# Performance work log

Hardware: AMD Instinct MI355X
Metric: run time of the kernel (lower is better)

Reference implementation:

```python
import jax, jax.numpy as jnp
import numpy as np

B, T, C, H = 2, 2048, 1024, 16
D = C // H  # head_dim = 64

def setup_inputs() -> dict:
    key = jax.random.key(0)
    k0, k1, k2, k3, k4 = jax.random.split(key, 5)
    s = 1.0 / np.sqrt(C)
    return {
        "x": jax.random.normal(k0, (B, T, C), dtype=jnp.float32),
        "w_qkv": jax.random.uniform(k1, (C, 3 * C), jnp.float32, -s, s),
        "b_qkv": jax.random.uniform(k2, (3 * C,), jnp.float32, -s, s),
        "w_proj": jax.random.uniform(k3, (C, C), jnp.float32, -s, s),
        "b_proj": jax.random.uniform(k4, (C,), jnp.float32, -s, s),
    }

def reference(x, w_qkv, b_qkv, w_proj, b_proj):
    Bx, Tx, Cx = x.shape
    qkv = x @ w_qkv + b_qkv                      # [B,T,3C]
    q, k, v = jnp.split(qkv, 3, axis=-1)
    # [B,T,C] -> [B,H,T,D]
    def heads(t):
        return t.reshape(Bx, Tx, H, D).transpose(0, 2, 1, 3)
    q, k, v = heads(q), heads(k), heads(v)
    att = jnp.einsum('bhqd,bhkd->bhqk', q, k) / np.sqrt(D).astype(np.float32)
    causal = jnp.tril(jnp.ones((Tx, Tx), dtype=bool))
    att = jnp.where(causal, att, -jnp.inf)
    att = jax.nn.softmax(att, axis=-1)
    y = jnp.einsum('bhqk,bhkd->bhqd', att, v)    # [B,H,T,D]
    y = y.transpose(0, 2, 1, 3).reshape(Bx, Tx, Cx)
    return y @ w_proj + b_proj
```

## Files before the change

kernel.cpp:

```cpp
#include <hip/hip_runtime.h>

typedef short bf16x8 __attribute__((ext_vector_type(8)));
typedef float f32x4 __attribute__((ext_vector_type(4)));
typedef unsigned short u16;
typedef unsigned short u16x8 __attribute__((ext_vector_type(8)));
typedef unsigned short u16x4 __attribute__((ext_vector_type(4), may_alias));

__device__ __forceinline__ u16 f2bf(float f) {
    union { float f; unsigned u; } v; v.f = f;
    unsigned r = v.u + 0x7fffu + ((v.u >> 16) & 1u);
    return (u16)(r >> 16);
}
__device__ __forceinline__ u16 f2bf_rhu(float f) {
    union { float f; unsigned u; } v; v.f = f;
    return (u16)((v.u + 0x8000u) >> 16);
}

__device__ __forceinline__ void gld_lds16(const void* g, void* l) {
    __builtin_amdgcn_global_load_lds(
        (const __attribute__((address_space(1))) void*)g,
        (__attribute__((address_space(3))) void*)l, 16, 0, 0);
}

__global__ __launch_bounds__(256) void x_to_bf16(const float* __restrict__ in,
                                                 u16* __restrict__ out) {
    const int i = blockIdx.x * 256 + threadIdx.x;
    float4 a = ((const float4*)in)[i * 2];
    float4 b = ((const float4*)in)[i * 2 + 1];
    u16x8 h;
    h[0] = f2bf(a.x); h[1] = f2bf(a.y); h[2] = f2bf(a.z); h[3] = f2bf(a.w);
    h[4] = f2bf(b.x); h[5] = f2bf(b.y); h[6] = f2bf(b.z); h[7] = f2bf(b.w);
    *(u16x8*)(out + (size_t)i * 8) = h;
}

__global__ __launch_bounds__(256) void transpose_w(const float* __restrict__ in,
                                                   u16* __restrict__ out,
                                                   int K, int N) {
    __shared__ float tile[32][33];
    const int n0 = blockIdx.x * 32, k0 = blockIdx.y * 32;
    const int tx = threadIdx.x, ty = threadIdx.y;
#pragma unroll
    for (int i = 0; i < 32; i += 8)
        tile[ty + i][tx] = in[(size_t)(k0 + ty + i) * N + n0 + tx];
    __syncthreads();
#pragma unroll
    for (int i = 0; i < 32; i += 8)
        out[(size_t)(n0 + ty + i) * K + k0 + tx] = f2bf(tile[tx][ty + i]);
}

#define QSCALE 0.180336880f

template <int OUTMODE, int BN>
__global__ __launch_bounds__(256) void gemm_m97(
    const u16* __restrict__ A, const u16* __restrict__ Bt,
    const float* __restrict__ bias, float* __restrict__ Cf,
    u16* __restrict__ Qo, u16* __restrict__ Ko, u16* __restrict__ Vt,
    int M, int N, int K) {
    constexpr int NF = BN / 32;
    __shared__ __align__(16) u16 lA[128 * 64];
    __shared__ __align__(16) u16 lB[BN * 64];

    const int tid = threadIdx.x;
    const int lane = tid & 63, wid = tid >> 6;
    const int wr = wid >> 1, wc = wid & 1;
    const int fr = lane & 15, fq = lane >> 4;
    const int m0 = blockIdx.y * 128, n0 = blockIdx.x * BN;

    const int gsrc = (lane & 7) ^ (lane >> 3);
    const u16* gA0 = A + (size_t)(m0 + (tid >> 3)) * K + gsrc * 8;
    const u16* gB0 = Bt + (size_t)(n0 + (tid >> 3)) * K + gsrc * 8;
    u16* lAw = lA + wid * 512;
    u16* lBw = lB + wid * 512;

    const int r7 = fr & 7;
    const int gk[2] = { ((0 + fq) ^ r7) * 8, ((4 + fq) ^ r7) * 8 };

    f32x4 acc[4][NF];
#pragma unroll
    for (int m = 0; m < 4; m++)
#pragma unroll
        for (int n = 0; n < NF; n++)
#pragma unroll
            for (int r = 0; r < 4; r++) acc[m][n][r] = 0.f;

    for (int k0 = 0; k0 < K; k0 += 64) {
        __syncthreads();
#pragma unroll
        for (int c = 0; c < 4; c++)
            gld_lds16(gA0 + (size_t)(c * 32) * K + k0, lAw + c * 2048);
#pragma unroll
        for (int c = 0; c < BN / 32; c++)
            gld_lds16(gB0 + (size_t)(c * 32) * K + k0, lBw + c * 2048);
        __syncthreads();

#pragma unroll
        for (int kf = 0; kf < 2; kf++) {
            bf16x8 a[4], b[NF];
#pragma unroll
            for (int m = 0; m < 4; m++)
                a[m] = *(const bf16x8*)&lA[(wr * 64 + m * 16 + fr) * 64 + gk[kf]];
#pragma unroll
            for (int n = 0; n < NF; n++)
                b[n] = *(const bf16x8*)&lB[(wc * (BN / 2) + n * 16 + fr) * 64 + gk[kf]];
#pragma unroll
            for (int m = 0; m < 4; m++)
#pragma unroll
                for (int n = 0; n < NF; n++)
                    acc[m][n] = __builtin_amdgcn_mfma_f32_16x16x32_bf16(a[m], b[n], acc[m][n], 0, 0, 0);
        }
    }

#pragma unroll
    for (int m = 0; m < 4; m++) {
#pragma unroll
        for (int n = 0; n < NF; n++) {
            const int row0 = m0 + wr * 64 + m * 16 + fq * 4;
            const int col = n0 + wc * (BN / 2) + n * 16 + fr;
            float v4[4];
#pragma unroll
            for (int r = 0; r < 4; r++) v4[r] = acc[m][n][r] + bias[col];
            if (OUTMODE == 0) {
                const int bb = row0 >> 11, t0 = row0 & 2047;
                const int sec = col >> 10, cc = col & 1023;
                const int h = cc >> 6, d = cc & 63;
                if (sec == 0) {
#pragma unroll
                    for (int r = 0; r < 4; r++)
                        Qo[(((size_t)(bb * 16 + h) * 2048 + t0 + r) << 6) + d] = f2bf(v4[r] * QSCALE);
                } else if (sec == 1) {
#pragma unroll
                    for (int r = 0; r < 4; r++)
                        Ko[(((size_t)(bb * 16 + h) * 2048 + t0 + r) << 6) + d] = f2bf(v4[r]);
                } else {
                    ushort4 p;
                    p.x = f2bf(v4[0]); p.y = f2bf(v4[1]); p.z = f2bf(v4[2]); p.w = f2bf(v4[3]);
                    *(ushort4*)&Vt[(((size_t)(bb * 16 + h) * 64 + d) << 11) + t0] = p;
                }
            } else {
#pragma unroll
                for (int r = 0; r < 4; r++)
                    Cf[(size_t)(row0 + r) * N + col] = v4[r];
            }
        }
    }
}

__global__ __launch_bounds__(256) void attn_kernel(const u16* __restrict__ Q,
                                                   const u16* __restrict__ Kg,
                                                   const u16* __restrict__ Vt,
                                                   u16* __restrict__ O) {
    __shared__ __align__(16) u16 lK[2][64 * 64];
    __shared__ __align__(16) u16 lV[2][64 * 64];
    __shared__ __align__(16) u16 lP[4][16 * 64];

    const int tid = threadIdx.x;
    const int lane = tid & 63, wid = tid >> 6;
    const int fr = lane & 15, fq = lane >> 4;
    const int bh = blockIdx.x & 31;
    const int qi = 31 - (blockIdx.x >> 5);
    const int qb0 = qi * 64;
    const size_t base = (size_t)bh * (2048 * 64);
    const u16* Qp = Q + base;
    const u16* Kp = Kg + base;
    const u16* Vp = Vt + base;

    const int q0 = qb0 + wid * 16;
    bf16x8 qa[2];
#pragma unroll
    for (int kf = 0; kf < 2; kf++)
        qa[kf] = *(const bf16x8*)&Qp[(size_t)(q0 + fr) * 64 + kf * 32 + fq * 8];
    asm volatile("s_waitcnt vmcnt(0)" ::: "memory");

    bf16x8 vones;
#pragma unroll
    for (int j = 0; j < 8; j++) vones[j] = (short)0x3F80;

    f32x4 o[4], lsum;
#pragma unroll
    for (int r = 0; r < 4; r++) {
        lsum[r] = 0.f;
#pragma unroll
        for (int n = 0; n < 4; n++) o[n][r] = 0.f;
    }

    const int srow0 = wid * 8 + (lane >> 3);
    const int gsrc = (lane & 7) ^ (lane >> 3);
    const u16* kSrc0 = Kp + (size_t)srow0 * 64 + gsrc * 8;
    const u16* vSrc0 = Vp + ((size_t)srow0 << 11) + gsrc * 8;

    const int r7 = fr & 7;
    const int gk0 = ((0 + fq) ^ r7) * 8;
    const int gk1 = ((4 + fq) ^ r7) * 8;

    const int pw_base = fr * 64 + (fq & 1) * 4;
    const int pw_gx = (fq >> 1);

    const int nt = qi + 1;

#define STAGE(buf, kt0_)                                                        \
    do {                                                                        \
        const int _kt0 = (kt0_);                                                \
        u16* _lkw = &lK[buf][wid * 512];                                        \
        u16* _lvw = &lV[buf][wid * 512];                                        \
        gld_lds16(kSrc0 + (size_t)_kt0 * 64, _lkw);                             \
        gld_lds16(kSrc0 + (size_t)(_kt0 + 32) * 64, _lkw + 2048);               \
        gld_lds16(vSrc0 + _kt0, _lvw);                                          \
        gld_lds16(vSrc0 + ((size_t)32 << 11) + _kt0, _lvw + 2048);              \
    } while (0)

    STAGE(0, 0);

    for (int kt = 0; kt < nt; kt++) {
        const int cur = kt & 1;
        if (kt + 1 < nt) {
            STAGE(cur ^ 1, (kt + 1) << 6);
            asm volatile("s_waitcnt vmcnt(4)" ::: "memory");
        } else {
            asm volatile("s_waitcnt vmcnt(0)" ::: "memory");
        }
        __builtin_amdgcn_s_barrier();

        const int kt0 = kt << 6;
        const u16* lKc = lK[cur];
        const u16* lVc = lV[cur];

        f32x4 s[4];
#pragma unroll
        for (int n = 0; n < 4; n++)
#pragma unroll
            for (int r = 0; r < 4; r++) s[n][r] = 0.f;
        __builtin_amdgcn_s_setprio(1);
#pragma unroll
        for (int n = 0; n < 4; n++) {
            bf16x8 kb0 = *(const bf16x8*)&lKc[(n * 16 + fr) * 64 + gk0];
            bf16x8 kb1 = *(const bf16x8*)&lKc[(n * 16 + fr) * 64 + gk1];
            s[n] = __builtin_amdgcn_mfma_f32_16x16x32_bf16(kb0, qa[0], s[n], 0, 0, 0);
            s[n] = __builtin_amdgcn_mfma_f32_16x16x32_bf16(kb1, qa[1], s[n], 0, 0, 0);
        }
        __builtin_amdgcn_s_setprio(0);

        if (kt == nt - 1) {
            const int qg = q0 + fr;
#pragma unroll
            for (int n = 0; n < 4; n++) {
                const int kg0 = kt0 + n * 16 + fq * 4;
#pragma unroll
                for (int r = 0; r < 4; r++)
                    if (kg0 + r > qg) s[n][r] = -200.f;
            }
        }

#pragma unroll
        for (int n = 0; n < 4; n++) {
            u16x4 w;
            w[0] = f2bf_rhu(__builtin_amdgcn_exp2f(s[n][0]));
            w[1] = f2bf_rhu(__builtin_amdgcn_exp2f(s[n][1]));
            w[2] = f2bf_rhu(__builtin_amdgcn_exp2f(s[n][2]));
            w[3] = f2bf_rhu(__builtin_amdgcn_exp2f(s[n][3]));
            const int g = ((2 * n + pw_gx) ^ r7) * 8;
            *(u16x4*)&lP[wid][pw_base + g] = w;
        }
        asm volatile("" ::: "memory");

        __builtin_amdgcn_s_setprio(1);
#pragma unroll
        for (int kf = 0; kf < 2; kf++) {
            const int gv = (kf == 0) ? gk0 : gk1;
            bf16x8 pb = *(const bf16x8*)&lP[wid][fr * 64 + gv];
            lsum = __builtin_amdgcn_mfma_f32_16x16x32_bf16(vones, pb, lsum, 0, 0, 0);
#pragma unroll
            for (int n = 0; n < 4; n++) {
                bf16x8 va = *(const bf16x8*)&lVc[(n * 16 + fr) * 64 + gv];
                o[n] = __builtin_amdgcn_mfma_f32_16x16x32_bf16(va, pb, o[n], 0, 0, 0);
            }
        }
        __builtin_amdgcn_s_setprio(0);

        __builtin_amdgcn_s_barrier();
    }
#undef STAGE

    const int bb = bh >> 4, hh = bh & 15;
    const float inv = 1.f / lsum[0];
    u16* orow = O + ((size_t)(bb * 2048 + q0 + fr)) * 1024 + hh * 64 + fq * 4;
#pragma unroll
    for (int n = 0; n < 4; n++) {
        ushort4 h;
        h.x = f2bf(o[n][0] * inv);
        h.y = f2bf(o[n][1] * inv);
        h.z = f2bf(o[n][2] * inv);
        h.w = f2bf(o[n][3] * inv);
        *(ushort4*)&orow[n * 16] = h;
    }
}

extern "C" void kernel_launch(void* const* d_in, const int* in_sizes, int n_in,
                              void* d_out, int out_size, void* d_ws, size_t ws_size,
                              hipStream_t stream) {
    const float* x      = (const float*)d_in[0];
    const float* w_qkv  = (const float*)d_in[1];
    const float* b_qkv  = (const float*)d_in[2];
    const float* w_proj = (const float*)d_in[3];
    const float* b_proj = (const float*)d_in[4];
    float* out = (float*)d_out;

    u16* ws = (u16*)d_ws;
    u16* wqkvT  = ws;
    u16* wprojT = wqkvT + 3072 * 1024;
    u16* Qb     = wprojT + 1024 * 1024;
    u16* Kb     = Qb + 32 * 2048 * 64;
    u16* Vtb    = Kb + 32 * 2048 * 64;
    u16* xb     = Vtb + 32 * 2048 * 64;
    u16* attnO  = xb;

    x_to_bf16<<<2048, 256, 0, stream>>>(x, xb);
    transpose_w<<<dim3(96, 32), dim3(32, 8), 0, stream>>>(w_qkv, wqkvT, 1024, 3072);
    transpose_w<<<dim3(32, 32), dim3(32, 8), 0, stream>>>(w_proj, wprojT, 1024, 1024);

    gemm_m97<0, 128><<<dim3(24, 32), 256, 0, stream>>>(
        xb, wqkvT, b_qkv, nullptr, Qb, Kb, Vtb, 4096, 3072, 1024);

    attn_kernel<<<1024, 256, 0, stream>>>(Qb, Kb, Vtb, attnO);

    gemm_m97<1, 64><<<dim3(16, 32), 256, 0, stream>>>(
        attnO, wprojT, b_proj, out, nullptr, nullptr, nullptr, 4096, 1024, 1024);
}
```

Measured before the change: 105.3 us.

## Merge prep kernels and split attention waves 2x2 over query and key halves

Fuses the x conversion and the two weight transposes into one prep launch, removing two kernel launches. Reworks the attention wave layout so each wave handles 32 queries against 32 keys of the tile instead of 16 queries against all 64 keys. K fragments are reused across two query groups, and partial outputs from the two key halves are combined through LDS at the end. It also sets launch_bounds occupancy to 4 blocks per CU. The cost is more registers per wave, an extra barrier and an LDS reduction, and the exp/softmax work stays the same.

```diff
diff --git a/kernel.cpp b/kernel.cpp
--- a/kernel.cpp
+++ b/kernel.cpp
@@ -5,6 +5,7 @@
 typedef unsigned short u16;
 typedef unsigned short u16x8 __attribute__((ext_vector_type(8)));
 typedef unsigned short u16x4 __attribute__((ext_vector_type(4), may_alias));
+typedef float f32x4_a __attribute__((ext_vector_type(4), may_alias));
 
 __device__ __forceinline__ u16 f2bf(float f) {
     union { float f; unsigned u; } v; v.f = f;
@@ -22,30 +23,35 @@
         (__attribute__((address_space(3))) void*)l, 16, 0, 0);
 }
 
-__global__ __launch_bounds__(256) void x_to_bf16(const float* __restrict__ in,
-                                                 u16* __restrict__ out) {
-    const int i = blockIdx.x * 256 + threadIdx.x;
-    float4 a = ((const float4*)in)[i * 2];
-    float4 b = ((const float4*)in)[i * 2 + 1];
-    u16x8 h;
-    h[0] = f2bf(a.x); h[1] = f2bf(a.y); h[2] = f2bf(a.z); h[3] = f2bf(a.w);
-    h[4] = f2bf(b.x); h[5] = f2bf(b.y); h[6] = f2bf(b.z); h[7] = f2bf(b.w);
-    *(u16x8*)(out + (size_t)i * 8) = h;
-}
-
-__global__ __launch_bounds__(256) void transpose_w(const float* __restrict__ in,
-                                                   u16* __restrict__ out,
-                                                   int K, int N) {
+__global__ __launch_bounds__(256) void prep_kernel(
+    const float* __restrict__ x, u16* __restrict__ xb,
+    const float* __restrict__ w_qkv, u16* __restrict__ wqkvT,
+    const float* __restrict__ w_proj, u16* __restrict__ wprojT) {
     __shared__ float tile[32][33];
-    const int n0 = blockIdx.x * 32, k0 = blockIdx.y * 32;
-    const int tx = threadIdx.x, ty = threadIdx.y;
+    const int b = blockIdx.x, tid = threadIdx.x;
+    if (b < 2048) {
+        const int i = b * 256 + tid;
+        float4 a = ((const float4*)x)[i * 2];
+        float4 c = ((const float4*)x)[i * 2 + 1];
+        u16x8 h;
+        h[0] = f2bf(a.x); h[1] = f2bf(a.y); h[2] = f2bf(a.z); h[3] = f2bf(a.w);
+        h[4] = f2bf(c.x); h[5] = f2bf(c.y); h[6] = f2bf(c.z); h[7] = f2bf(c.w);
+        *(u16x8*)(xb + (size_t)i * 8) = h;
+        return;
+    }
+    const float* in; u16* out; int N, bx;
+    if (b < 5120) { bx = b - 2048; in = w_qkv; out = wqkvT; N = 3072; }
+    else          { bx = b - 5120; in = w_proj; out = wprojT; N = 1024; }
+    const int nblk = N / 32;
+    const int n0 = (bx % nblk) * 32, k0 = (bx / nblk) * 32;
+    const int tx = tid & 31, ty = tid >> 5;
 #pragma unroll
     for (int i = 0; i < 32; i += 8)
         tile[ty + i][tx] = in[(size_t)(k0 + ty + i) * N + n0 + tx];
     __syncthreads();
 #pragma unroll
     for (int i = 0; i < 32; i += 8)
-        out[(size_t)(n0 + ty + i) * K + k0 + tx] = f2bf(tile[tx][ty + i]);
+        out[(size_t)(n0 + ty + i) * 1024 + k0 + tx] = f2bf(tile[tx][ty + i]);
 }
 
 #define QSCALE 0.180336880f
@@ -145,17 +151,18 @@
     }
 }
 
-__global__ __launch_bounds__(256) void attn_kernel(const u16* __restrict__ Q,
-                                                   const u16* __restrict__ Kg,
-                                                   const u16* __restrict__ Vt,
-                                                   u16* __restrict__ O) {
+__global__ __launch_bounds__(256, 4) void attn_kernel(const u16* __restrict__ Q,
+                                                      const u16* __restrict__ Kg,
+                                                      const u16* __restrict__ Vt,
+                                                      u16* __restrict__ O) {
     __shared__ __align__(16) u16 lK[2][64 * 64];
     __shared__ __align__(16) u16 lV[2][64 * 64];
-    __shared__ __align__(16) u16 lP[4][16 * 64];
+    __shared__ __align__(16) u16 lP[4][32 * 32];
 
     const int tid = threadIdx.x;
     const int lane = tid & 63, wid = tid >> 6;
     const int fr = lane & 15, fq = lane >> 4;
+    const int kw = wid >> 1, qw = wid & 1;
     const int bh = blockIdx.x & 31;
     const int qi = 31 - (blockIdx.x >> 5);
     const int qb0 = qi * 64;
@@ -164,23 +171,28 @@
     const u16* Kp = Kg + base;
     const u16* Vp = Vt + base;
 
-    const int q0 = qb0 + wid * 16;
-    bf16x8 qa[2];
-#pragma unroll
-    for (int kf = 0; kf < 2; kf++)
-        qa[kf] = *(const bf16x8*)&Qp[(size_t)(q0 + fr) * 64 + kf * 32 + fq * 8];
+    const int q0w = qb0 + qw * 32;
+    bf16x8 qa[2][2];
+#pragma unroll
+    for (int qg = 0; qg < 2; qg++)
+#pragma unroll
+        for (int kf = 0; kf < 2; kf++)
+            qa[qg][kf] = *(const bf16x8*)&Qp[(size_t)(q0w + qg * 16 + fr) * 64 + kf * 32 + fq * 8];
     asm volatile("s_waitcnt vmcnt(0)" ::: "memory");
 
     bf16x8 vones;
 #pragma unroll
     for (int j = 0; j < 8; j++) vones[j] = (short)0x3F80;
 
-    f32x4 o[4], lsum;
-#pragma unroll
-    for (int r = 0; r < 4; r++) {
-        lsum[r] = 0.f;
-#pragma unroll
-        for (int n = 0; n < 4; n++) o[n][r] = 0.f;
+    f32x4 o[4][2], lsum[2];
+#pragma unroll
+    for (int qg = 0; qg < 2; qg++) {
+#pragma unroll
+        for (int r = 0; r < 4; r++) lsum[qg][r] = 0.f;
+#pragma unroll
+        for (int dg = 0; dg < 4; dg++)
+#pragma unroll
+            for (int r = 0; r < 4; r++) o[dg][qg][r] = 0.f;
     }
 
     const int srow0 = wid * 8 + (lane >> 3);
@@ -191,9 +203,7 @@
     const int r7 = fr & 7;
     const int gk0 = ((0 + fq) ^ r7) * 8;
     const int gk1 = ((4 + fq) ^ r7) * 8;
-
-    const int pw_base = fr * 64 + (fq & 1) * 4;
-    const int pw_gx = (fq >> 1);
+    const int gkv = ((kw * 4 + fq) ^ r7) * 8;
 
     const int nt = qi + 1;
 
@@ -224,55 +234,69 @@
         const u16* lKc = lK[cur];
         const u16* lVc = lV[cur];
 
-        f32x4 s[4];
-#pragma unroll
-        for (int n = 0; n < 4; n++)
-#pragma unroll
-            for (int r = 0; r < 4; r++) s[n][r] = 0.f;
+        f32x4 s[2][2];
+#pragma unroll
+        for (int kg = 0; kg < 2; kg++)
+#pragma unroll
+            for (int qg = 0; qg < 2; qg++)
+#pragma unroll
+                for (int r = 0; r < 4; r++) s[kg][qg][r] = 0.f;
         __builtin_amdgcn_s_setprio(1);
 #pragma unroll
-        for (int n = 0; n < 4; n++) {
-            bf16x8 kb0 = *(const bf16x8*)&lKc[(n * 16 + fr) * 64 + gk0];
-            bf16x8 kb1 = *(const bf16x8*)&lKc[(n * 16 + fr) * 64 + gk1];
-            s[n] = __builtin_amdgcn_mfma_f32_16x16x32_bf16(kb0, qa[0], s[n], 0, 0, 0);
-            s[n] = __builtin_amdgcn_mfma_f32_16x16x32_bf16(kb1, qa[1], s[n], 0, 0, 0);
+        for (int kg = 0; kg < 2; kg++) {
+            const int krow = (kw * 32 + kg * 16 + fr) * 64;
+            bf16x8 kb0 = *(const bf16x8*)&lKc[krow + gk0];
+            bf16x8 kb1 = *(const bf16x8*)&lKc[krow + gk1];
+#pragma unroll
+            for (int qg = 0; qg < 2; qg++) {
+                s[kg][qg] = __builtin_amdgcn_mfma_f32_16x16x32_bf16(kb0, qa[qg][0], s[kg][qg], 0, 0, 0);
+                s[kg][qg] = __builtin_amdgcn_mfma_f32_16x16x32_bf16(kb1, qa[qg][1], s[kg][qg], 0, 0, 0);
+            }
         }
         __builtin_amdgcn_s_setprio(0);
 
         if (kt == nt - 1) {
-            const int qg = q0 + fr;
-#pragma unroll
-            for (int n = 0; n < 4; n++) {
-                const int kg0 = kt0 + n * 16 + fq * 4;
-#pragma unroll
-                for (int r = 0; r < 4; r++)
-                    if (kg0 + r > qg) s[n][r] = -200.f;
-            }
-        }
-
-#pragma unroll
-        for (int n = 0; n < 4; n++) {
-            u16x4 w;
-            w[0] = f2bf_rhu(__builtin_amdgcn_exp2f(s[n][0]));
-            w[1] = f2bf_rhu(__builtin_amdgcn_exp2f(s[n][1]));
-            w[2] = f2bf_rhu(__builtin_amdgcn_exp2f(s[n][2]));
-            w[3] = f2bf_rhu(__builtin_amdgcn_exp2f(s[n][3]));
-            const int g = ((2 * n + pw_gx) ^ r7) * 8;
-            *(u16x4*)&lP[wid][pw_base + g] = w;
-        }
+#pragma unroll
+            for (int kg = 0; kg < 2; kg++) {
+                const int kg0 = kt0 + kw * 32 + kg * 16 + fq * 4;
+#pragma unroll
+                for (int qg = 0; qg < 2; qg++) {
+                    const int qg0 = q0w + qg * 16 + fr;
+#pragma unroll
+                    for (int r = 0; r < 4; r++)
+                        if (kg0 + r > qg0) s[kg][qg][r] = -200.f;
+                }
+            }
+        }
+
+#pragma unroll
+        for (int kg = 0; kg < 2; kg++)
+#pragma unroll
+            for (int qg = 0; qg < 2; qg++) {
+                const int ql = qg * 16 + fr;
+                u16x4 w;
+                w[0] = f2bf_rhu(__builtin_amdgcn_exp2f(s[kg][qg][0]));
+                w[1] = f2bf_rhu(__builtin_amdgcn_exp2f(s[kg][qg][1]));
+                w[2] = f2bf_rhu(__builtin_amdgcn_exp2f(s[kg][qg][2]));
+                w[3] = f2bf_rhu(__builtin_amdgcn_exp2f(s[kg][qg][3]));
+                const int g = (kg * 2 + (fq >> 1)) ^ (ql & 3);
+                *(u16x4*)&lP[wid][ql * 32 + g * 8 + (fq & 1) * 4] = w;
+            }
         asm volatile("" ::: "memory");
 
         __builtin_amdgcn_s_setprio(1);
-#pragma unroll
-        for (int kf = 0; kf < 2; kf++) {
-            const int gv = (kf == 0) ? gk0 : gk1;
-            bf16x8 pb = *(const bf16x8*)&lP[wid][fr * 64 + gv];
-            lsum = __builtin_amdgcn_mfma_f32_16x16x32_bf16(vones, pb, lsum, 0, 0, 0);
-#pragma unroll
-            for (int n = 0; n < 4; n++) {
-                bf16x8 va = *(const bf16x8*)&lVc[(n * 16 + fr) * 64 + gv];
-                o[n] = __builtin_amdgcn_mfma_f32_16x16x32_bf16(va, pb, o[n], 0, 0, 0);
-            }
+        bf16x8 va[4];
+#pragma unroll
+        for (int dg = 0; dg < 4; dg++)
+            va[dg] = *(const bf16x8*)&lVc[(dg * 16 + fr) * 64 + gkv];
+#pragma unroll
+        for (int qg = 0; qg < 2; qg++) {
+            const int ql = qg * 16 + fr;
+            bf16x8 pb = *(const bf16x8*)&lP[wid][ql * 32 + (fq ^ (ql & 3)) * 8];
+            lsum[qg] = __builtin_amdgcn_mfma_f32_16x16x32_bf16(vones, pb, lsum[qg], 0, 0, 0);
+#pragma unroll
+            for (int dg = 0; dg < 4; dg++)
+                o[dg][qg] = __builtin_amdgcn_mfma_f32_16x16x32_bf16(va[dg], pb, o[dg][qg], 0, 0, 0);
         }
         __builtin_amdgcn_s_setprio(0);
 
@@ -280,17 +304,49 @@
     }
 #undef STAGE
 
-    const int bb = bh >> 4, hh = bh & 15;
-    const float inv = 1.f / lsum[0];
-    u16* orow = O + ((size_t)(bb * 2048 + q0 + fr)) * 1024 + hh * 64 + fq * 4;
-#pragma unroll
-    for (int n = 0; n < 4; n++) {
-        ushort4 h;
-        h.x = f2bf(o[n][0] * inv);
-        h.y = f2bf(o[n][1] * inv);
-        h.z = f2bf(o[n][2] * inv);
-        h.w = f2bf(o[n][3] * inv);
-        *(ushort4*)&orow[n * 16] = h;
+    float* cmb = (float*)&lK[0][0];
+    float* slab = cmb + (size_t)qw * 2560 + lane * 40;
+    if (kw == 1) {
+#pragma unroll
+        for (int dg = 0; dg < 4; dg++)
+#pragma unroll
+            for (int qg = 0; qg < 2; qg++)
+                *(f32x4_a*)&slab[(dg * 2 + qg) * 4] = o[dg][qg];
+#pragma unroll
+        for (int qg = 0; qg < 2; qg++)
+            *(f32x4_a*)&slab[32 + qg * 4] = lsum[qg];
+    }
+    __syncthreads();
+    if (kw == 0) {
+#pragma unroll
+        for (int dg = 0; dg < 4; dg++)
+#pragma unroll
+            for (int qg = 0; qg < 2; qg++) {
+                f32x4_a p = *(const f32x4_a*)&slab[(dg * 2 + qg) * 4];
+#pragma unroll
+                for (int r = 0; r < 4; r++) o[dg][qg][r] += p[r];
+            }
+#pragma unroll
+        for (int qg = 0; qg < 2; qg++) {
+            f32x4_a p = *(const f32x4_a*)&slab[32 + qg * 4];
+            lsum[qg][0] += p[0];
+        }
+
+        const int bb = bh >> 4, hh = bh & 15;
+#pragma unroll
+        for (int qg = 0; qg < 2; qg++) {
+            const float inv = 1.f / lsum[qg][0];
+            u16* orow = O + ((size_t)(bb * 2048 + q0w + qg * 16 + fr)) * 1024 + hh * 64 + fq * 4;
+#pragma unroll
+            for (int dg = 0; dg < 4; dg++) {
+                ushort4 h;
+                h.x = f2bf(o[dg][qg][0] * inv);
+                h.y = f2bf(o[dg][qg][1] * inv);
+                h.z = f2bf(o[dg][qg][2] * inv);
+                h.w = f2bf(o[dg][qg][3] * inv);
+                *(ushort4*)&orow[dg * 16] = h;
+            }
+        }
     }
 }
 
@@ -313,9 +369,7 @@
     u16* xb     = Vtb + 32 * 2048 * 64;
     u16* attnO  = xb;
 
-    x_to_bf16<<<2048, 256, 0, stream>>>(x, xb);
-    transpose_w<<<dim3(96, 32), dim3(32, 8), 0, stream>>>(w_qkv, wqkvT, 1024, 3072);
-    transpose_w<<<dim3(32, 32), dim3(32, 8), 0, stream>>>(w_proj, wprojT, 1024, 1024);
+    prep_kernel<<<6144, 256, 0, stream>>>(x, xb, w_qkv, wqkvT, w_proj, wprojT);
 
     gemm_m97<0, 128><<<dim3(24, 32), 256, 0, stream>>>(
         xb, wqkvT, b_qkv, nullptr, Qb, Kb, Vtb, 4096, 3072, 1024);
```

After: 98.71 us. -6.2%, faster.
